# Performance work log

Hardware: AMD Instinct MI355X
Metric: run time of the kernel (lower is better)

Reference implementation:

```python
import jax, jax.numpy as jnp
import numpy as np
from jax import lax

NUM_CLASSES = 21
MAX_OUT = 5          # max_output_size in tf.image.non_max_suppression
IOU_THR = 0.5        # NMS_IOU_THRESHOLD
CONF_THR = 0.5       # CONFIDENCE_THRESHOLD
NEG = -1e9           # stand-in for -inf score (suppressed / background)


def setup_inputs() -> dict:
    key = jax.random.key(0)
    k1, k2, k3 = jax.random.split(key, 3)
    B, N, C = 128, 8732, NUM_CLASSES
    logits = jax.random.normal(k1, (B, N, 4 + C), dtype=jnp.float32)
    # default boxes in corner format [ymin, xmin, ymax, xmax], valid geometry
    ctr = jax.random.uniform(k2, (N, 2), dtype=jnp.float32)                 # cy, cx
    sz = jax.random.uniform(k3, (N, 2), dtype=jnp.float32, minval=0.05, maxval=0.3)  # h, w
    default_boxes = jnp.clip(
        jnp.concatenate([ctr - sz / 2, ctr + sz / 2], axis=-1), 0.0, 1.0)
    return {"logits": logits, "default_boxes": default_boxes}


def _decode(loc, db):
    # db: [N,4] corners -> center/size (matches get_offset's tf.stack)
    cy = (db[:, 2] + db[:, 0]) / 2
    cx = (db[:, 3] + db[:, 1]) / 2
    h = db[:, 2] - db[:, 0]
    w = db[:, 3] - db[:, 1]
    # loc: [B,N,4] = (dy, dx, dh, dw)
    ncy = loc[..., 0] * h + cy
    ncx = loc[..., 1] * w + cx
    nh = jnp.exp(loc[..., 2]) * h
    nw = jnp.exp(loc[..., 3]) * w
    boxes = jnp.stack(
        [ncy - nh / 2, ncx - nw / 2, ncy + nh / 2, ncx + nw / 2], axis=-1)
    return jnp.clip(boxes, 0.0, 1.0)


def _iou_one_vs_all(box, boxes):
    # box [4], boxes [N,4], corner format
    tl = jnp.maximum(box[:2], boxes[:, :2])
    br = jnp.minimum(box[2:], boxes[:, 2:])
    wh = jnp.maximum(br - tl, 0.0)
    inter = wh[:, 0] * wh[:, 1]
    a1 = (box[2] - box[0]) * (box[3] - box[1])
    a2 = (boxes[:, 2] - boxes[:, 0]) * (boxes[:, 3] - boxes[:, 1])
    return inter / (a1 + a2 - inter + 1e-12)


def _nms_single(boxes, scores, classes_f):
    # boxes [N,4], scores [N] (background already set to NEG), classes_f [N] float
    def step(s, _):
        i = jnp.argmax(s)
        sc = s[i]
        b = boxes[i]
        valid = sc > CONF_THR  # score_threshold in tf NMS
        iou = _iou_one_vs_all(b, boxes)
        s = jnp.where(iou > IOU_THR, NEG, s)  # suppresses i too (IoU=1)
        return s, (b, classes_f[i], sc, valid)

    _, (bs, cs, ss, vs) = lax.scan(step, scores, None, length=MAX_OUT)
    # pad invalid slots with zeros (TF returns variable-length; we use fixed 5 + zero pad)
    bs = jnp.where(vs[:, None], bs, 0.0)
    cs = jnp.where(vs, cs, 0.0)
    ss = jnp.where(vs, ss, 0.0)
    return bs, cs[:, None], ss[:, None]  # [5,4], [5,1], [5,1]


def reference(logits, default_boxes):
    boxes = _decode(logits[..., :4], default_boxes)          # [B,N,4]
    probs = jax.nn.softmax(logits[..., 4:], axis=-1)         # [B,N,C]
    scores = jnp.max(probs, axis=-1)                          # [B,N]
    classes = jnp.argmax(probs, axis=-1)                      # [B,N] int
    # boolean_mask(classes != 0) expressed as score = -inf for background
    scores_eff = jnp.where(classes != 0, scores, NEG)
    det_b, det_c, det_s = jax.vmap(_nms_single)(
        boxes, scores_eff, classes.astype(jnp.float32))
    # pack detection_boxes / detection_classes / detection_scores -> [B,5,6]
    return jnp.concatenate([det_b, det_c, det_s], axis=-1)
```

## Files before the change

kernel.cpp:

```cpp
#include <hip/hip_runtime.h>

#define NEG (-1e9f)
constexpr int NCLS   = 21;
constexpr int NBOX   = 8732;
constexpr int MAXOUT = 5;
constexpr int CAP    = NBOX;
constexpr float IOU_THR  = 0.5f;
constexpr float CONF_THR = 0.5f;

constexpr int TPB             = 128;
constexpr int BOXES_PER_BLOCK = TPB * 4;
constexpr int BPB             = (NBOX + BOXES_PER_BLOCK - 1) / BOXES_PER_BLOCK;

using u64 = unsigned long long;
typedef float f4_t __attribute__((ext_vector_type(4)));


__device__ __forceinline__ u64 pk2(float a, float b) {
    union { float f[2]; u64 u; } x; x.f[0] = a; x.f[1] = b; return x.u;
}
__device__ __forceinline__ float lo2(u64 u) { union { u64 v; float f[2]; } x; x.v = u; return x.f[0]; }
__device__ __forceinline__ float hi2(u64 u) { union { u64 v; float f[2]; } x; x.v = u; return x.f[1]; }

__device__ __forceinline__ void ast(u64* p, u64 v) {
    __hip_atomic_store(p, v, __ATOMIC_RELAXED, __HIP_MEMORY_SCOPE_AGENT);
}
__device__ __forceinline__ u64 ald(const u64* p) {
    return __hip_atomic_load(p, __ATOMIC_RELAXED, __HIP_MEMORY_SCOPE_AGENT);
}

__device__ __forceinline__ void process_box(
        const float* __restrict__ v,
        int b, int n, f4_t db,
        u64* __restrict__ cand,
        int* __restrict__ cnt) {
    float cy = (db[2] + db[0]) * 0.5f;
    float cx = (db[3] + db[1]) * 0.5f;
    float h  = db[2] - db[0];
    float w  = db[3] - db[1];
    float ncy = v[0] * h + cy;
    float ncx = v[1] * w + cx;
    float nh  = expf(v[2]) * h;
    float nw  = expf(v[3]) * w;
    float y1 = fminf(fmaxf(ncy - nh * 0.5f, 0.f), 1.f);
    float x1 = fminf(fmaxf(ncx - nw * 0.5f, 0.f), 1.f);
    float y2 = fminf(fmaxf(ncy + nh * 0.5f, 0.f), 1.f);
    float x2 = fminf(fmaxf(ncx + nw * 0.5f, 0.f), 1.f);

    float m = v[4];
    int am = 0;
#pragma unroll
    for (int j = 1; j < NCLS; j++) {
        float x = v[4 + j];
        if (x > m) { m = x; am = j; }
    }
    float sum = 0.f;
#pragma unroll
    for (int j = 0; j < NCLS; j++) sum += expf(v[4 + j] - m);
    float score = 1.0f / sum;

    if (am != 0 && score > CONF_THR) {
        int p = atomicAdd(&cnt[b], 1);
        if (p < CAP) {
            u64* c = cand + ((long long)b * CAP + p) * 4;
            ast(c + 0, pk2(y1, x1));
            ast(c + 1, pk2(y2, x2));
            ast(c + 2, pk2(score, (float)n));
            ast(c + 3, pk2((float)am, 0.f));
        }
    }
}

__global__ __launch_bounds__(TPB, 3) void fused_kernel(
        const float* __restrict__ logits,
        const float4* __restrict__ dbox4,
        u64* __restrict__ cand,
        int* __restrict__ cnt,
        int* __restrict__ done,
        float* __restrict__ out) {
    const int b   = blockIdx.x / BPB;
    const int blk = blockIdx.x % BPB;
    const int n0  = blk * BOXES_PER_BLOCK + threadIdx.x * 4;

    __shared__ int s_last;

    if (n0 < NBOX) {
        const f4_t* f4  = (const f4_t*)(logits + ((long long)b * NBOX + n0) * 25);
        const f4_t* dbp = (const f4_t*)dbox4;

        f4_t r[25];
#pragma unroll
        for (int k = 0; k < 25; k++) r[k] = f4[k];
        f4_t d0 = dbp[n0 + 0], d1 = dbp[n0 + 1], d2 = dbp[n0 + 2], d3 = dbp[n0 + 3];

        asm volatile(""
            : "+v"(r[0]), "+v"(r[1]), "+v"(r[2]), "+v"(r[3]), "+v"(r[4]),
              "+v"(r[5]), "+v"(r[6]), "+v"(r[7]), "+v"(r[8]), "+v"(r[9]),
              "+v"(r[10]), "+v"(r[11]), "+v"(r[12]));
        asm volatile(""
            : "+v"(r[13]), "+v"(r[14]), "+v"(r[15]), "+v"(r[16]), "+v"(r[17]),
              "+v"(r[18]), "+v"(r[19]), "+v"(r[20]), "+v"(r[21]), "+v"(r[22]),
              "+v"(r[23]), "+v"(r[24]), "+v"(d0), "+v"(d1), "+v"(d2), "+v"(d3));

        float v[100];
#pragma unroll
        for (int k = 0; k < 25; k++) {
            v[4 * k + 0] = r[k][0]; v[4 * k + 1] = r[k][1];
            v[4 * k + 2] = r[k][2]; v[4 * k + 3] = r[k][3];
        }
        process_box(v + 0,  b, n0 + 0, d0, cand, cnt);
        process_box(v + 25, b, n0 + 1, d1, cand, cnt);
        process_box(v + 50, b, n0 + 2, d2, cand, cnt);
        process_box(v + 75, b, n0 + 3, d3, cand, cnt);
    }

    __syncthreads();
    if (threadIdx.x == 0)
        s_last = (__hip_atomic_fetch_add(&done[b], 1, __ATOMIC_RELAXED,
                                         __HIP_MEMORY_SCOPE_AGENT) == BPB - 1);
    __syncthreads();
    if (!s_last) return;
    if (threadIdx.x >= 64) return;

    const int lane = threadIdx.x;
    const int M = min((int)__hip_atomic_load(&cnt[b], __ATOMIC_RELAXED,
                                             __HIP_MEMORY_SCOPE_AGENT), CAP);
    const u64* cb = cand + (long long)b * CAP * 4;
    float* o = out + (long long)b * MAXOUT * 6;

    int k = 0;
    if (M <= 64) {
        float sc = -INFINITY, oid = 3.0e38f;
        float y1 = 0.f, x1 = 0.f, y2 = 0.f, x2 = 0.f, cls = 0.f;
        if (lane < M) {
            const u64* c = cb + (long long)lane * 4;
            u64 w0 = ald(c + 0), w1 = ald(c + 1), w2 = ald(c + 2), w3 = ald(c + 3);
            y1 = lo2(w0); x1 = hi2(w0);
            y2 = lo2(w1); x2 = hi2(w1);
            sc = lo2(w2); oid = hi2(w2);
            cls = lo2(w3);
        }
        for (; k < MAXOUT; k++) {
            float bv = sc, boid = oid;
            int bi = (lane < M) ? lane : -1;
            for (int mm = 32; mm >= 1; mm >>= 1) {
                float v2 = __shfl_xor(bv,   mm, 64);
                float o2 = __shfl_xor(boid, mm, 64);
                int   i2 = __shfl_xor(bi,   mm, 64);
                if (v2 > bv || (v2 == bv && o2 < boid)) { bv = v2; boid = o2; bi = i2; }
            }
            if (bi < 0 || !(bv > CONF_THR)) break;

            float sy1 = __shfl(y1, bi, 64), sx1 = __shfl(x1, bi, 64);
            float sy2 = __shfl(y2, bi, 64), sx2 = __shfl(x2, bi, 64);
            float scl = __shfl(cls, bi, 64);
            if (lane == 0) {
                o[k * 6 + 0] = sy1; o[k * 6 + 1] = sx1;
                o[k * 6 + 2] = sy2; o[k * 6 + 3] = sx2;
                o[k * 6 + 4] = scl; o[k * 6 + 5] = bv;
            }
            float a1 = (sy2 - sy1) * (sx2 - sx1);
            float tly = fmaxf(sy1, y1);
            float tlx = fmaxf(sx1, x1);
            float bry = fminf(sy2, y2);
            float brx = fminf(sx2, x2);
            float wh0 = fmaxf(bry - tly, 0.f);
            float wh1 = fmaxf(brx - tlx, 0.f);
            float inter = wh0 * wh1;
            float a2 = (y2 - y1) * (x2 - x1);
            float iou = inter / (a1 + a2 - inter + 1e-12f);
            if (lane < M && iou > IOU_THR) sc = NEG;
        }
    } else {
        for (; k < MAXOUT; k++) {
            float bv = -INFINITY, boid = 3.0e38f;
            int bi = -1;
            for (int i = lane; i < M; i += 64) {
                u64 w2 = ald(cb + (long long)i * 4 + 2);
                float v = lo2(w2), od = hi2(w2);
                if (v > bv || (v == bv && od < boid)) { bv = v; boid = od; bi = i; }
            }
            for (int mm = 32; mm >= 1; mm >>= 1) {
                float v2 = __shfl_xor(bv,   mm, 64);
                float o2 = __shfl_xor(boid, mm, 64);
                int   i2 = __shfl_xor(bi,   mm, 64);
                if (v2 > bv || (v2 == bv && o2 < boid)) { bv = v2; boid = o2; bi = i2; }
            }
            if (bi < 0 || !(bv > CONF_THR)) break;

            u64 sw0 = ald(cb + (long long)bi * 4 + 0);
            u64 sw1 = ald(cb + (long long)bi * 4 + 1);
            float sy1 = lo2(sw0), sx1 = hi2(sw0), sy2 = lo2(sw1), sx2 = hi2(sw1);
            if (lane == 0) {
                u64 sw3 = ald(cb + (long long)bi * 4 + 3);
                o[k * 6 + 0] = sy1; o[k * 6 + 1] = sx1;
                o[k * 6 + 2] = sy2; o[k * 6 + 3] = sx2;
                o[k * 6 + 4] = lo2(sw3); o[k * 6 + 5] = bv;
            }
            float a1 = (sy2 - sy1) * (sx2 - sx1);
            for (int i = lane; i < M; i += 64) {
                u64 w0 = ald(cb + (long long)i * 4 + 0);
                u64 w1 = ald(cb + (long long)i * 4 + 1);
                float cy1 = lo2(w0), cx1 = hi2(w0), cy2 = lo2(w1), cx2 = hi2(w1);
                float tly = fmaxf(sy1, cy1);
                float tlx = fmaxf(sx1, cx1);
                float bry = fminf(sy2, cy2);
                float brx = fminf(sx2, cx2);
                float wh0 = fmaxf(bry - tly, 0.f);
                float wh1 = fmaxf(brx - tlx, 0.f);
                float inter = wh0 * wh1;
                float a2 = (cy2 - cy1) * (cx2 - cx1);
                float iou = inter / (a1 + a2 - inter + 1e-12f);
                if (iou > IOU_THR) {
                    u64 w2 = ald(cb + (long long)i * 4 + 2);
                    ast((u64*)(cb + (long long)i * 4 + 2), pk2(NEG, hi2(w2)));
                }
            }
        }
    }
    for (int j = k * 6 + lane; j < MAXOUT * 6; j += 64) o[j] = 0.f;
}

extern "C" void kernel_launch(void* const* d_in, const int* in_sizes, int n_in,
                              void* d_out, int out_size, void* d_ws, size_t ws_size,
                              hipStream_t stream) {
    const float* logits = (const float*)d_in[0];
    const float4* dbox4 = (const float4*)d_in[1];
    float* out          = (float*)d_out;

    const int N = in_sizes[1] / 4;
    const int B = in_sizes[0] / (N * 25);

    int* cnt  = (int*)d_ws;
    int* done = cnt + B;
    u64* cand = (u64*)((char*)d_ws +
        ((2 * (size_t)B * sizeof(int) + 15) & ~(size_t)15));

    hipMemsetAsync(d_ws, 0, 2 * (size_t)B * sizeof(int), stream);
    fused_kernel<<<B * BPB, TPB, 0, stream>>>(logits, dbox4, cand, cnt, done, out);
}
```

Before: 190.5 us.

## Stage logits tile into LDS via direct global-to-LDS loads

Replaces per-thread strided 100-byte vector loads of logits with coalesced 16-byte global_load_lds transfers that fill a 51KB shared tile per block, then each thread reads its four boxes from LDS. This targets uncoalesced global access, since each thread previously read a separate 100-byte span. The cost is much larger LDS usage per block, which limits occupancy; the min-3-blocks launch bound is dropped, and LDS reads at a 100-float stride may cause bank conflicts.

Result: slower. 197.8 us (+3.8%).

```diff
diff --git a/kernel.cpp b/kernel.cpp
--- a/kernel.cpp
+++ b/kernel.cpp
@@ -11,6 +11,8 @@
 constexpr int TPB             = 128;
 constexpr int BOXES_PER_BLOCK = TPB * 4;
 constexpr int BPB             = (NBOX + BOXES_PER_BLOCK - 1) / BOXES_PER_BLOCK;
+constexpr int TILE_BYTES      = BOXES_PER_BLOCK * 100;
+constexpr int TILE_FLOATS     = TILE_BYTES / 4;
 
 using u64 = unsigned long long;
 typedef float f4_t __attribute__((ext_vector_type(4)));
@@ -27,6 +29,13 @@
 }
 __device__ __forceinline__ u64 ald(const u64* p) {
     return __hip_atomic_load(p, __ATOMIC_RELAXED, __HIP_MEMORY_SCOPE_AGENT);
+}
+
+__device__ __forceinline__ void gload_lds16(const void* g, void* l) {
+    __builtin_amdgcn_global_load_lds(
+        (const __attribute__((address_space(1))) void*)g,
+        (__attribute__((address_space(3))) void*)l,
+        16, 0, 0);
 }
 
 __device__ __forceinline__ void process_box(
@@ -71,47 +80,53 @@
     }
 }
 
-__global__ __launch_bounds__(TPB, 3) void fused_kernel(
+__global__ __launch_bounds__(TPB) void fused_kernel(
         const float* __restrict__ logits,
         const float4* __restrict__ dbox4,
         u64* __restrict__ cand,
         int* __restrict__ cnt,
         int* __restrict__ done,
         float* __restrict__ out) {
-    const int b   = blockIdx.x / BPB;
-    const int blk = blockIdx.x % BPB;
-    const int n0  = blk * BOXES_PER_BLOCK + threadIdx.x * 4;
-
+    const int b    = blockIdx.x / BPB;
+    const int blk  = blockIdx.x % BPB;
+    const int wave = threadIdx.x >> 6;
+    const int lane = threadIdx.x & 63;
+
+    __shared__ __align__(16) float tile[TILE_FLOATS];
     __shared__ int s_last;
 
+    const int box0   = blk * BOXES_PER_BLOCK;
+    const int nboxes = min(BOXES_PER_BLOCK, NBOX - box0);
+    const int bytes  = nboxes * 100;
+    const int ninstr = (bytes + 1023) >> 10;
+
+    const char* gbase =
+        (const char*)logits + ((long long)b * NBOX + box0) * 100;
+
+    for (int j = wave; j < ninstr; j += 2) {
+        int off = j * 1024 + lane * 16;
+        off = min(off, bytes - 16);
+        gload_lds16(gbase + off, (char*)tile + (j * 1024));
+    }
+    __syncthreads();
+
+    const int t  = threadIdx.x;
+    const int n0 = box0 + t * 4;
     if (n0 < NBOX) {
-        const f4_t* f4  = (const f4_t*)(logits + ((long long)b * NBOX + n0) * 25);
+        const f4_t* lt  = (const f4_t*)(tile + t * 100);
         const f4_t* dbp = (const f4_t*)dbox4;
-
-        f4_t r[25];
-#pragma unroll
-        for (int k = 0; k < 25; k++) r[k] = f4[k];
-        f4_t d0 = dbp[n0 + 0], d1 = dbp[n0 + 1], d2 = dbp[n0 + 2], d3 = dbp[n0 + 3];
-
-        asm volatile(""
-            : "+v"(r[0]), "+v"(r[1]), "+v"(r[2]), "+v"(r[3]), "+v"(r[4]),
-              "+v"(r[5]), "+v"(r[6]), "+v"(r[7]), "+v"(r[8]), "+v"(r[9]),
-              "+v"(r[10]), "+v"(r[11]), "+v"(r[12]));
-        asm volatile(""
-            : "+v"(r[13]), "+v"(r[14]), "+v"(r[15]), "+v"(r[16]), "+v"(r[17]),
-              "+v"(r[18]), "+v"(r[19]), "+v"(r[20]), "+v"(r[21]), "+v"(r[22]),
-              "+v"(r[23]), "+v"(r[24]), "+v"(d0), "+v"(d1), "+v"(d2), "+v"(d3));
 
         float v[100];
 #pragma unroll
         for (int k = 0; k < 25; k++) {
-            v[4 * k + 0] = r[k][0]; v[4 * k + 1] = r[k][1];
-            v[4 * k + 2] = r[k][2]; v[4 * k + 3] = r[k][3];
-        }
-        process_box(v + 0,  b, n0 + 0, d0, cand, cnt);
-        process_box(v + 25, b, n0 + 1, d1, cand, cnt);
-        process_box(v + 50, b, n0 + 2, d2, cand, cnt);
-        process_box(v + 75, b, n0 + 3, d3, cand, cnt);
+            f4_t r = lt[k];
+            v[4 * k + 0] = r[0]; v[4 * k + 1] = r[1];
+            v[4 * k + 2] = r[2]; v[4 * k + 3] = r[3];
+        }
+        process_box(v + 0,  b, n0 + 0, dbp[n0 + 0], cand, cnt);
+        process_box(v + 25, b, n0 + 1, dbp[n0 + 1], cand, cnt);
+        process_box(v + 50, b, n0 + 2, dbp[n0 + 2], cand, cnt);
+        process_box(v + 75, b, n0 + 3, dbp[n0 + 3], cand, cnt);
     }
 
     __syncthreads();
@@ -122,7 +137,6 @@
     if (!s_last) return;
     if (threadIdx.x >= 64) return;
 
-    const int lane = threadIdx.x;
     const int M = min((int)__hip_atomic_load(&cnt[b], __ATOMIC_RELAXED,
                                              __HIP_MEMORY_SCOPE_AGENT), CAP);
     const u64* cb = cand + (long long)b * CAP * 4;
```
